# Kernel optimization log

Measured on AMD Instinct MI355X. Metric: run time of the kernel, lower is better.

Reference implementation:

```python
import jax, jax.numpy as jnp
import numpy as np

D_MODEL = 768
N_HEADS = 12
D_FF = 3072
EPS = 1e-5


def _dense_params(key, d_in, d_out):
    kw, kb = jax.random.split(key)
    bound = 1.0 / np.sqrt(d_in)
    W = jax.random.uniform(kw, (d_in, d_out), minval=-bound, maxval=bound, dtype=jnp.float32)
    b = jax.random.uniform(kb, (d_out,), minval=-bound, maxval=bound, dtype=jnp.float32)
    return W, b


def setup_inputs() -> dict:
    key = jax.random.key(0)
    ks = jax.random.split(key, 8)
    x = jax.random.normal(ks[0], (2, 2048, D_MODEL), dtype=jnp.float32)
    wq, bq = _dense_params(ks[1], D_MODEL, D_MODEL)
    wk, bk = _dense_params(ks[2], D_MODEL, D_MODEL)
    wv, bv = _dense_params(ks[3], D_MODEL, D_MODEL)
    wo, bo = _dense_params(ks[4], D_MODEL, D_MODEL)
    w1, b1 = _dense_params(ks[5], D_MODEL, D_FF)
    w2, b2 = _dense_params(ks[6], D_FF, D_MODEL)
    g1 = jnp.ones((D_MODEL,), jnp.float32); be1 = jnp.zeros((D_MODEL,), jnp.float32)
    g2 = jnp.ones((D_MODEL,), jnp.float32); be2 = jnp.zeros((D_MODEL,), jnp.float32)
    return {"x": x, "wq": wq, "bq": bq, "wk": wk, "bk": bk, "wv": wv, "bv": bv,
            "wo": wo, "bo": bo, "w1": w1, "b1": b1, "w2": w2, "b2": b2,
            "g1": g1, "be1": be1, "g2": g2, "be2": be2}


def _layernorm(x, g, b):
    mu = jnp.mean(x, axis=-1, keepdims=True)
    var = jnp.mean(jnp.square(x - mu), axis=-1, keepdims=True)
    return (x - mu) * jax.lax.rsqrt(var + EPS) * g + b


def reference(x, wq, bq, wk, bk, wv, bv, wo, bo, w1, b1, w2, b2, g1, be1, g2, be2):
    B, S, D = x.shape
    H, dk = N_HEADS, D // N_HEADS
    # projections -> [B, H, S, dk]
    def split_heads(t):
        return t.reshape(B, S, H, dk).transpose(0, 2, 1, 3)
    q = split_heads(x @ wq + bq)
    k = split_heads(x @ wk + bk)
    v = split_heads(x @ wv + bv)
    scores = jnp.einsum('bhqd,bhkd->bhqk', q, k) / np.sqrt(dk).astype(np.float32)
    causal = jnp.tril(jnp.ones((S, S), dtype=bool))  # True = keep
    scores = jnp.where(causal, scores, -jnp.inf)
    attn = jax.nn.softmax(scores, axis=-1)
    out = jnp.einsum('bhqk,bhkd->bhqd', attn, v)
    out = out.transpose(0, 2, 1, 3).reshape(B, S, D)
    attn_out = out @ wo + bo
    x = _layernorm(x + attn_out, g1, be1)
    ff = jax.nn.relu(x @ w1 + b1) @ w2 + b2
    x = _layernorm(x + ff, g2, be2)
    return x
```

## Files before the change

### kernel.cpp

```cpp
#include <hip/hip_runtime.h>
#include <stdint.h>

#define S_LEN 2048
#define BATCH 2
#define DM 768
#define NH 12
#define DKH 64
#define DFF 3072
#define MROWS (BATCH * S_LEN)

typedef short bf16x8 __attribute__((ext_vector_type(8)));
typedef float f32x4 __attribute__((ext_vector_type(4)));
typedef float f32x16 __attribute__((ext_vector_type(16)));

__device__ __forceinline__ unsigned short f2b(float f) {
    union { float f; unsigned u; } cv; cv.f = f;
    unsigned u = cv.u;
    unsigned r = (u + 0x7FFFu + ((u >> 16) & 1u)) >> 16;
    return (unsigned short)r;
}

__device__ __forceinline__ void gload16(const void* g, void* l) {
    __builtin_amdgcn_global_load_lds(
        (const __attribute__((address_space(1))) unsigned int*)g,
        (__attribute__((address_space(3))) unsigned int*)l, 16, 0, 0);
}

__device__ __forceinline__ unsigned cvtpk(float lo, float hi) {
    unsigned r;
    asm("v_cvt_pk_bf16_f32 %0, %1, %2" : "=v"(r) : "v"(lo), "v"(hi));
    return r;
}
__device__ __forceinline__ void pswap(unsigned &a, unsigned &b) {
    asm("v_permlane32_swap_b32 %0, %1" : "+v"(a), "+v"(b));
}
__device__ __forceinline__ bf16x8 mkpa(unsigned w0, unsigned w1, unsigned w2, unsigned w3) {
    union { unsigned u[4]; bf16x8 h; } cv;
    cv.u[0] = w0; cv.u[1] = w1; cv.u[2] = w2; cv.u[3] = w3;
    return cv.h;
}

__global__ __launch_bounds__(256) void prep_kernel(
    const float* __restrict__ x,
    const float* __restrict__ wq, const float* __restrict__ wk,
    const float* __restrict__ wv, const float* __restrict__ wo,
    const float* __restrict__ w1, const float* __restrict__ w2,
    unsigned short* __restrict__ x16, unsigned short* __restrict__ wqkv16,
    unsigned short* __restrict__ wo16, unsigned short* __restrict__ w116,
    unsigned short* __restrict__ w216) {
    const int t = threadIdx.x;
    int bid = blockIdx.x;
    if (bid < 3072) {
        const int i = bid * 256 + t;
        float4 v = reinterpret_cast<const float4*>(x)[i];
        ushort4 o;
        o.x = f2b(v.x); o.y = f2b(v.y); o.z = f2b(v.z); o.w = f2b(v.w);
        reinterpret_cast<ushort4*>(x16)[i] = o;
        return;
    }
    bid -= 3072;
    const float* in; unsigned short* out; int R, C, bx, by;
    if (bid < 2304) {
        const int wsel = bid / 576, r = bid % 576;
        in = (wsel == 0) ? wq : (wsel == 1) ? wk : (wsel == 2) ? wv : wo;
        out = (wsel == 3) ? wo16 : wqkv16 + (size_t)wsel * DM * DM;
        R = DM; C = DM; bx = r % 24; by = r / 24;
    } else if (bid < 4608) {
        const int r = bid - 2304;
        in = w1; out = w116; R = DM; C = DFF; bx = r % 96; by = r / 96;
    } else {
        const int r = bid - 4608;
        in = w2; out = w216; R = DFF; C = DM; bx = r % 24; by = r / 24;
    }
    __shared__ float tile[32][33];
    const int c0 = bx * 32, r0 = by * 32;
    const int tx = t & 31, ty = t >> 5;
    #pragma unroll
    for (int i = ty; i < 32; i += 8)
        tile[i][tx] = in[(size_t)(r0 + i) * C + c0 + tx];
    __syncthreads();
    #pragma unroll
    for (int i = ty; i < 32; i += 8)
        out[(size_t)(c0 + i) * R + r0 + tx] = f2b(tile[tx][i]);
}

#define STG192(buf, kt)                                                                  \
    {                                                                                    \
        const char* ga = (const char*)(A + (size_t)bm * lda + koff + ((kt) << 6));       \
        const char* gb = (const char*)(Bt + (size_t)bn * ldb + koff + ((kt) << 6));      \
        char* la = (char*)Sh + (buf) * 57344 + t * 16;                                   \
        char* lb = (char*)Sh + (buf) * 57344 + 32768 + t * 16;                           \
        _Pragma("unroll")                                                                \
        for (int p = 0; p < 4; ++p)                                                      \
            gload16(ga + (size_t)(sr + p * 64) * la2 + scb_sw, la + p * 8192);           \
        _Pragma("unroll")                                                                \
        for (int p = 0; p < 3; ++p)                                                      \
            gload16(gb + (size_t)(sr + p * 64) * lb2 + scb_sw, lb + p * 8192);           \
    }

template <int EPI>
__global__ __launch_bounds__(512, 2) void gemm192(
    const unsigned short* __restrict__ A, int lda,
    const unsigned short* __restrict__ Bt, int ldb,
    const float* __restrict__ bias0, const float* __restrict__ bias1,
    const float* __restrict__ bias2,
    unsigned short* __restrict__ ob0, unsigned short* __restrict__ ob1,
    unsigned short* __restrict__ ob2, float* __restrict__ of,
    int M, int N, int Ksub, float qscale) {
    __shared__ __align__(16) unsigned short Sh[2 * 28672];
    const int t = threadIdx.x;
    const int wave = t >> 6, lane = t & 63;
    const int wr = wave >> 2, wc = wave & 3;
    const int bn = blockIdx.x * 192, bm = blockIdx.y * 256;
    const int koff = (EPI == 2) ? blockIdx.z * Ksub : 0;
    const int lr = lane & 15;
    const int lk8 = (lane >> 4) << 3;
    const int sr = t >> 3;
    const int scb = (t & 7) * 16;
    const int scb_sw = scb ^ ((sr & 7) << 4);
    const int swr = (lr & 7) << 4;
    const size_t la2 = (size_t)lda * 2, lb2 = (size_t)ldb * 2;

    f32x4 acc[8][3];
    #pragma unroll
    for (int i = 0; i < 8; ++i)
        #pragma unroll
        for (int j = 0; j < 3; ++j) { f32x4 z = {0.f, 0.f, 0.f, 0.f}; acc[i][j] = z; }

    const int nkt = Ksub >> 6;
    STG192(0, 0)
    for (int kt = 0; kt < nkt; ++kt) {
        const int cur = kt & 1;
        if (kt + 1 < nkt) {
            STG192(cur ^ 1, kt + 1)
            asm volatile("s_waitcnt vmcnt(7)" ::: "memory");
        } else {
            asm volatile("s_waitcnt vmcnt(0)" ::: "memory");
        }
        __builtin_amdgcn_s_barrier();
        __builtin_amdgcn_sched_barrier(0);
        const char* Ab = (const char*)Sh + cur * 57344;
        const char* Bb = Ab + 32768;
        #pragma unroll
        for (int ks = 0; ks < 64; ks += 32) {
            const int cbsw = ((ks + lk8) * 2) ^ swr;
            bf16x8 af[8], bfv[3];
            #pragma unroll
            for (int i = 0; i < 8; ++i)
                af[i] = *reinterpret_cast<const bf16x8*>(Ab + (wr * 128 + i * 16 + lr) * 128 + cbsw);
            #pragma unroll
            for (int j = 0; j < 3; ++j)
                bfv[j] = *reinterpret_cast<const bf16x8*>(Bb + (wc * 48 + j * 16 + lr) * 128 + cbsw);
            __builtin_amdgcn_s_setprio(1);
            #pragma unroll
            for (int i = 0; i < 8; ++i)
                #pragma unroll
                for (int j = 0; j < 3; ++j)
                    acc[i][j] = __builtin_amdgcn_mfma_f32_16x16x32_bf16(af[i], bfv[j], acc[i][j], 0, 0, 0);
            __builtin_amdgcn_s_setprio(0);
        }
        __builtin_amdgcn_s_barrier();
    }

    const int r0 = (lane >> 4) << 2;
    if (EPI == 0) {
        #pragma unroll
        for (int i = 0; i < 8; ++i) {
            const int row_b = bm + wr * 128 + i * 16 + r0;
            #pragma unroll
            for (int j = 0; j < 3; ++j) {
                const int col = bn + wc * 48 + j * 16 + lr;
                const float bvv = bias0[col];
                #pragma unroll
                for (int r = 0; r < 4; ++r) {
                    float vv = acc[i][j][r] + bvv;
                    vv = vv > 0.f ? vv : 0.f;
                    ob0[(size_t)(row_b + r) * N + col] = f2b(vv);
                }
            }
        }
    } else if (EPI == 1) {
        const int sec = (bn >= 2 * DM) ? 2 : (bn >= DM ? 1 : 0);
        const int nb = bn - sec * DM;
        const float* bias = (sec == 0) ? bias0 : (sec == 1 ? bias1 : bias2);
        #pragma unroll
        for (int i = 0; i < 8; ++i) {
            const int row_b = bm + wr * 128 + i * 16 + r0;
            const int b = row_b >> 11, s = row_b & 2047;
            #pragma unroll
            for (int j = 0; j < 3; ++j) {
                const int c768 = nb + wc * 48 + j * 16 + lr;
                const int h = c768 >> 6, d = c768 & 63;
                const float bvv = bias[c768];
                if (sec == 2) {
                    ushort4 w;
                    w.x = f2b(acc[i][j][0] + bvv);
                    w.y = f2b(acc[i][j][1] + bvv);
                    w.z = f2b(acc[i][j][2] + bvv);
                    w.w = f2b(acc[i][j][3] + bvv);
                    *reinterpret_cast<ushort4*>(
                        ob2 + (((size_t)(b * NH + h) * DKH) + d) * S_LEN + s) = w;
                } else {
                    const float sc = (sec == 0) ? qscale : 1.f;
                    unsigned short* dst = (sec == 0) ? ob0 : ob1;
                    #pragma unroll
                    for (int r = 0; r < 4; ++r)
                        dst[(((size_t)(b * NH + h) * S_LEN) + s + r) * DKH + d] =
                            f2b((acc[i][j][r] + bvv) * sc);
                }
            }
        }
    } else {
        float* op = of + (size_t)blockIdx.z * M * N;
        #pragma unroll
        for (int i = 0; i < 8; ++i) {
            const int row_b = bm + wr * 128 + i * 16 + r0;
            #pragma unroll
            for (int j = 0; j < 3; ++j) {
                const int col = bn + wc * 48 + j * 16 + lr;
                #pragma unroll
                for (int r = 0; r < 4; ++r)
                    op[(size_t)(row_b + r) * N + col] = acc[i][j][r];
            }
        }
    }
}

template <int RELU, int RES, int EF32, int EB16>
__global__ __launch_bounds__(256) void gemm_bt64(
    const unsigned short* __restrict__ A, const unsigned short* __restrict__ Bt,
    const float* __restrict__ bias, const float* __restrict__ res,
    float* __restrict__ outf, unsigned short* __restrict__ outb,
    int M, int N, int K) {
    __shared__ __align__(16) unsigned short As[128 * 64];
    __shared__ __align__(16) unsigned short Bs[64 * 64];
    const int t = threadIdx.x;
    const int wave = t >> 6, lane = t & 63;
    const int bn = blockIdx.x * 64, bm = blockIdx.y * 128;
    const int lr = lane & 15;
    const int lk8 = (lane >> 4) << 3;
    const int srow = t >> 3;
    const int scol = (t & 7) * 16;
    f32x4 acc[2][4];
    #pragma unroll
    for (int i = 0; i < 2; ++i)
        #pragma unroll
        for (int j = 0; j < 4; ++j) { f32x4 z = {0.f, 0.f, 0.f, 0.f}; acc[i][j] = z; }
    const int nkt = K >> 6;
    for (int kt = 0; kt < nkt; ++kt) {
        const char* ga = (const char*)(A + (size_t)bm * K + (kt << 6));
        const char* gb = (const char*)(Bt + (size_t)bn * K + (kt << 6));
        const size_t K2 = (size_t)K * 2;
        #pragma unroll
        for (int p = 0; p < 4; ++p)
            gload16(ga + (size_t)(srow + p * 32) * K2 + scol, (char*)As + p * 4096 + t * 16);
        #pragma unroll
        for (int p = 0; p < 2; ++p)
            gload16(gb + (size_t)(srow + p * 32) * K2 + scol, (char*)Bs + p * 4096 + t * 16);
        __syncthreads();
        #pragma unroll
        for (int ks = 0; ks < 64; ks += 32) {
            bf16x8 af[2], bfv[4];
            #pragma unroll
            for (int i = 0; i < 2; ++i)
                af[i] = *reinterpret_cast<const bf16x8*>(&As[(wave * 32 + i * 16 + lr) * 64 + ks + lk8]);
            #pragma unroll
            for (int j = 0; j < 4; ++j)
                bfv[j] = *reinterpret_cast<const bf16x8*>(&Bs[(j * 16 + lr) * 64 + ks + lk8]);
            #pragma unroll
            for (int i = 0; i < 2; ++i)
                #pragma unroll
                for (int j = 0; j < 4; ++j)
                    acc[i][j] = __builtin_amdgcn_mfma_f32_16x16x32_bf16(af[i], bfv[j], acc[i][j], 0, 0, 0);
        }
        __syncthreads();
    }
    const int r0 = (lane >> 4) << 2;
    #pragma unroll
    for (int i = 0; i < 2; ++i) {
        const int row_b = bm + wave * 32 + i * 16 + r0;
        #pragma unroll
        for (int j = 0; j < 4; ++j) {
            const int col = bn + j * 16 + lr;
            const float bvv = bias[col];
            #pragma unroll
            for (int r = 0; r < 4; ++r) {
                float vv = acc[i][j][r] + bvv;
                if (RES) vv += res[(size_t)(row_b + r) * N + col];
                if (RELU) vv = vv > 0.f ? vv : 0.f;
                if (EF32) outf[(size_t)(row_b + r) * N + col] = vv;
                if (EB16) outb[(size_t)(row_b + r) * N + col] = f2b(vv);
            }
        }
    }
}

#define ALOADK(dst, k0v)                                                     \
    _Pragma("unroll") for (int kh = 0; kh < 2; ++kh)                         \
        _Pragma("unroll") for (int c = 0; c < 4; ++c)                        \
            dst[kh][c] = *reinterpret_cast<const bf16x8*>(                   \
                kb + (size_t)((k0v) + kh * 32 + x) * DKH + c * 16 + k8);
#define ALOADV(dst, k0v)                                                     \
    _Pragma("unroll") for (int dt = 0; dt < 2; ++dt)                         \
        _Pragma("unroll") for (int s = 0; s < 4; ++s)                        \
            dst[dt][s] = *reinterpret_cast<const bf16x8*>(                   \
                vbg + (size_t)(dt * 32 + x) * S_LEN + (k0v) + s * 16 + k8);

__global__ __launch_bounds__(64) void attn_mfma_kernel(
    const unsigned short* __restrict__ q16,
    const unsigned short* __restrict__ k16,
    const unsigned short* __restrict__ vt16,
    unsigned short* __restrict__ ctx16) {
    const int lane = threadIdx.x & 63;
    const int bh = blockIdx.x;
    const int qb = (gridDim.y - 1) - blockIdx.y;
    const int b = bh / NH, h = bh % NH;
    const size_t hbase = (size_t)bh * S_LEN * DKH;
    const int x = lane & 31;
    const int hi = lane >> 5;
    const int k8 = hi << 3;
    const int sW = qb << 5;
    const int qg = sW + x;

    bf16x8 qa[4];
    #pragma unroll
    for (int c = 0; c < 4; ++c)
        qa[c] = *reinterpret_cast<const bf16x8*>(
            q16 + hbase + (size_t)(sW + x) * DKH + c * 16 + k8);

    float mst = -3e38f, lst = 0.f;
    f32x16 acc0, acc1;
    #pragma unroll
    for (int r = 0; r < 16; ++r) { acc0[r] = 0.f; acc1[r] = 0.f; }

    const unsigned short* kb = k16 + hbase;
    const unsigned short* vbg = vt16 + hbase;
    const int nt = (sW >> 6) + 1;

    bf16x8 kac[2][4];
    ALOADK(kac, 0)
    for (int kt = 0; kt < nt; ++kt) {
        const int k0 = kt << 6;
        bf16x8 vac[2][4];
        ALOADV(vac, k0)
        bf16x8 kan[2][4];
        if (kt + 1 < nt) { ALOADK(kan, k0 + 64) }

        f32x16 sc0, sc1;
        #pragma unroll
        for (int r = 0; r < 16; ++r) { sc0[r] = 0.f; sc1[r] = 0.f; }
        __builtin_amdgcn_s_setprio(1);
        #pragma unroll
        for (int c = 0; c < 4; ++c) {
            sc0 = __builtin_amdgcn_mfma_f32_32x32x16_bf16(kac[0][c], qa[c], sc0, 0, 0, 0);
            sc1 = __builtin_amdgcn_mfma_f32_32x32x16_bf16(kac[1][c], qa[c], sc1, 0, 0, 0);
        }
        __builtin_amdgcn_s_setprio(0);

        if (kt == nt - 1) {
            #pragma unroll
            for (int r = 0; r < 16; ++r) {
                const int cr = (r & 3) + (hi << 2) + ((r >> 2) << 3);
                if (k0 + cr > qg) sc0[r] = -3e38f;
                if (k0 + 32 + cr > qg) sc1[r] = -3e38f;
            }
        }

        float tm = fmaxf(sc0[0], sc0[1]);
        #pragma unroll
        for (int r = 2; r < 16; ++r) tm = fmaxf(tm, sc0[r]);
        #pragma unroll
        for (int r = 0; r < 16; ++r) tm = fmaxf(tm, sc1[r]);
        tm = fmaxf(tm, __shfl_xor(tm, 32));

        if (!__all(tm <= mst + 8.f)) {
            const float mn = fmaxf(mst, tm);
            const float corr = exp2f(mst - mn);
            mst = mn;
            lst *= corr;
            float cw[16];
            #pragma unroll
            for (int r = 0; r < 16; ++r)
                cw[r] = __shfl(corr, (r & 3) + (hi << 2) + ((r >> 2) << 3));
            #pragma unroll
            for (int r = 0; r < 16; ++r) { acc0[r] *= cw[r]; acc1[r] *= cw[r]; }
        }

        float ts = 0.f;
        #pragma unroll
        for (int r = 0; r < 16; ++r) {
            sc0[r] = exp2f(sc0[r] - mst); ts += sc0[r];
            sc1[r] = exp2f(sc1[r] - mst); ts += sc1[r];
        }
        ts += __shfl_xor(ts, 32);
        lst += ts;

        unsigned a0 = cvtpk(sc0[0], sc0[1]),   b0 = cvtpk(sc0[4], sc0[5]);   pswap(a0, b0);
        unsigned a1 = cvtpk(sc0[2], sc0[3]),   b1 = cvtpk(sc0[6], sc0[7]);   pswap(a1, b1);
        unsigned a2 = cvtpk(sc0[8], sc0[9]),   b2 = cvtpk(sc0[12], sc0[13]); pswap(a2, b2);
        unsigned a3 = cvtpk(sc0[10], sc0[11]), b3 = cvtpk(sc0[14], sc0[15]); pswap(a3, b3);
        bf16x8 pa00 = mkpa(a0, a1, b0, b1);
        bf16x8 pa01 = mkpa(a2, a3, b2, b3);
        unsigned c0 = cvtpk(sc1[0], sc1[1]),   d0 = cvtpk(sc1[4], sc1[5]);   pswap(c0, d0);
        unsigned c1 = cvtpk(sc1[2], sc1[3]),   d1 = cvtpk(sc1[6], sc1[7]);   pswap(c1, d1);
        unsigned c2 = cvtpk(sc1[8], sc1[9]),   d2 = cvtpk(sc1[12], sc1[13]); pswap(c2, d2);
        unsigned c3 = cvtpk(sc1[10], sc1[11]), d3 = cvtpk(sc1[14], sc1[15]); pswap(c3, d3);
        bf16x8 pa10 = mkpa(c0, c1, d0, d1);
        bf16x8 pa11 = mkpa(c2, c3, d2, d3);

        __builtin_amdgcn_s_setprio(1);
        acc0 = __builtin_amdgcn_mfma_f32_32x32x16_bf16(pa00, vac[0][0], acc0, 0, 0, 0);
        acc1 = __builtin_amdgcn_mfma_f32_32x32x16_bf16(pa00, vac[1][0], acc1, 0, 0, 0);
        acc0 = __builtin_amdgcn_mfma_f32_32x32x16_bf16(pa01, vac[0][1], acc0, 0, 0, 0);
        acc1 = __builtin_amdgcn_mfma_f32_32x32x16_bf16(pa01, vac[1][1], acc1, 0, 0, 0);
        acc0 = __builtin_amdgcn_mfma_f32_32x32x16_bf16(pa10, vac[0][2], acc0, 0, 0, 0);
        acc1 = __builtin_amdgcn_mfma_f32_32x32x16_bf16(pa10, vac[1][2], acc1, 0, 0, 0);
        acc0 = __builtin_amdgcn_mfma_f32_32x32x16_bf16(pa11, vac[0][3], acc0, 0, 0, 0);
        acc1 = __builtin_amdgcn_mfma_f32_32x32x16_bf16(pa11, vac[1][3], acc1, 0, 0, 0);
        __builtin_amdgcn_s_setprio(0);

        if (kt + 1 < nt) {
            #pragma unroll
            for (int kh = 0; kh < 2; ++kh)
                #pragma unroll
                for (int c = 0; c < 4; ++c) kac[kh][c] = kan[kh][c];
        }
    }

    const float li = 1.f / lst;
    float lw[16];
    #pragma unroll
    for (int r = 0; r < 16; ++r)
        lw[r] = __shfl(li, (r & 3) + (hi << 2) + ((r >> 2) << 3));
    #pragma unroll
    for (int r = 0; r < 16; ++r) {
        const int q = sW + (r & 3) + (hi << 2) + ((r >> 2) << 3);
        const size_t rowb = ((size_t)b * S_LEN + q) * DM + h * DKH;
        ctx16[rowb + x] = f2b(acc0[r] * lw[r]);
        ctx16[rowb + 32 + x] = f2b(acc1[r] * lw[r]);
    }
}

template <int EB16>
__global__ __launch_bounds__(256) void layernorm_kernel(
    const float* __restrict__ in, const float* __restrict__ gam, const float* __restrict__ bet,
    float* __restrict__ outf, unsigned short* __restrict__ outb) {
    __shared__ float red[8];
    const int row = blockIdx.x, t = threadIdx.x;
    const int wave = t >> 6, lane = t & 63;
    const float* p = in + (size_t)row * DM;
    const float v0 = p[t], v1 = p[t + 256], v2 = p[t + 512];
    float s = v0 + v1 + v2;
    float sq = v0 * v0 + v1 * v1 + v2 * v2;
    #pragma unroll
    for (int off = 32; off > 0; off >>= 1) { s += __shfl_xor(s, off); sq += __shfl_xor(sq, off); }
    if (lane == 0) { red[wave] = s; red[wave + 4] = sq; }
    __syncthreads();
    s = red[0] + red[1] + red[2] + red[3];
    sq = red[4] + red[5] + red[6] + red[7];
    const float mu = s * (1.f / DM);
    const float var = sq * (1.f / DM) - mu * mu;
    const float rs = rsqrtf(var + 1e-5f);
    #pragma unroll
    for (int i = 0; i < 3; ++i) {
        const int c = t + i * 256;
        const float vv = (i == 0 ? v0 : (i == 1 ? v1 : v2));
        const float y = (vv - mu) * rs * gam[c] + bet[c];
        outf[(size_t)row * DM + c] = y;
        if (EB16) outb[(size_t)row * DM + c] = f2b(y);
    }
}

template <int EB16>
__global__ __launch_bounds__(192) void ln_merge_kernel(
    const float* __restrict__ part, size_t pstride, int ns,
    const float* __restrict__ res, const float* __restrict__ bias,
    const float* __restrict__ gam, const float* __restrict__ bet,
    float* __restrict__ outf, unsigned short* __restrict__ outb) {
    __shared__ float red[8];
    const int row = blockIdx.x, t = threadIdx.x;
    const int wave = t >> 6, lane = t & 63;
    const size_t base = (size_t)row * DM;
    float4 v = reinterpret_cast<const float4*>(res + base)[t];
    const float4 bv = reinterpret_cast<const float4*>(bias)[t];
    v.x += bv.x; v.y += bv.y; v.z += bv.z; v.w += bv.w;
    for (int z = 0; z < ns; ++z) {
        const float4 p = reinterpret_cast<const float4*>(part + (size_t)z * pstride + base)[t];
        v.x += p.x; v.y += p.y; v.z += p.z; v.w += p.w;
    }
    float s = v.x + v.y + v.z + v.w;
    float sq = v.x * v.x + v.y * v.y + v.z * v.z + v.w * v.w;
    #pragma unroll
    for (int off = 32; off > 0; off >>= 1) { s += __shfl_xor(s, off); sq += __shfl_xor(sq, off); }
    if (lane == 0) { red[wave] = s; red[wave + 4] = sq; }
    __syncthreads();
    s = red[0] + red[1] + red[2];
    sq = red[4] + red[5] + red[6];
    const float mu = s * (1.f / DM);
    const float var = sq * (1.f / DM) - mu * mu;
    const float rs = rsqrtf(var + 1e-5f);
    const float4 g = reinterpret_cast<const float4*>(gam)[t];
    const float4 be = reinterpret_cast<const float4*>(bet)[t];
    float4 o;
    o.x = (v.x - mu) * rs * g.x + be.x;
    o.y = (v.y - mu) * rs * g.y + be.y;
    o.z = (v.z - mu) * rs * g.z + be.z;
    o.w = (v.w - mu) * rs * g.w + be.w;
    reinterpret_cast<float4*>(outf + base)[t] = o;
    if (EB16) {
        ushort4 ob;
        ob.x = f2b(o.x); ob.y = f2b(o.y); ob.z = f2b(o.z); ob.w = f2b(o.w);
        reinterpret_cast<ushort4*>(outb + base)[t] = ob;
    }
}

extern "C" void kernel_launch(void* const* d_in, const int* in_sizes, int n_in,
                              void* d_out, int out_size, void* d_ws, size_t ws_size,
                              hipStream_t stream) {
    const float* x   = (const float*)d_in[0];
    const float* wq  = (const float*)d_in[1];
    const float* bq  = (const float*)d_in[2];
    const float* wk  = (const float*)d_in[3];
    const float* bk  = (const float*)d_in[4];
    const float* wv  = (const float*)d_in[5];
    const float* bv  = (const float*)d_in[6];
    const float* wo  = (const float*)d_in[7];
    const float* bo  = (const float*)d_in[8];
    const float* w1  = (const float*)d_in[9];
    const float* b1  = (const float*)d_in[10];
    const float* w2  = (const float*)d_in[11];
    const float* b2  = (const float*)d_in[12];
    const float* g1  = (const float*)d_in[13];
    const float* be1 = (const float*)d_in[14];
    const float* g2  = (const float*)d_in[15];
    const float* be2 = (const float*)d_in[16];

    char* wp = (char*)d_ws;
    auto alloc = [&](size_t bytes) -> void* {
        void* r = (void*)wp;
        wp += (bytes + 255) & ~(size_t)255;
        return r;
    };
    const int M = MROWS;
    unsigned short* wqkv16 = (unsigned short*)alloc((size_t)3 * DM * DM * 2);
    unsigned short* wo16 = (unsigned short*)alloc((size_t)DM * DM * 2);
    unsigned short* w116 = (unsigned short*)alloc((size_t)DM * DFF * 2);
    unsigned short* w216 = (unsigned short*)alloc((size_t)DM * DFF * 2);
    unsigned short* ctx16 = (unsigned short*)alloc((size_t)M * DM * 2);
    float* y1 = (float*)alloc((size_t)M * DM * 4);
    unsigned short* x16  = (unsigned short*)alloc((size_t)M * DM * 2);
    unsigned short* q16  = (unsigned short*)alloc((size_t)M * DM * 2);
    unsigned short* k16  = (unsigned short*)alloc((size_t)M * DM * 2);
    unsigned short* vt16 = (unsigned short*)alloc((size_t)M * DM * 2);
    unsigned short* ff116 = x16;
    unsigned short* x116  = ctx16;

    const size_t per = (size_t)M * DM * 4;
    size_t used = (size_t)(wp - (char*)d_ws);
    int NS = 1;
    if (used + 4 * per + 1024 <= ws_size) NS = 4;
    else if (used + 2 * per + 1024 <= ws_size) NS = 2;
    float* part = (float*)alloc((size_t)NS * per);

    prep_kernel<<<9984, 256, 0, stream>>>(x, wq, wk, wv, wo, w1, w2,
                                          x16, wqkv16, wo16, w116, w216);

    const float QSCALE = 0.125f * 1.44269504088896f;
    gemm192<1><<<dim3(3 * DM / 192, M / 256), 512, 0, stream>>>(
        x16, DM, wqkv16, DM, bq, bk, bv, q16, k16, vt16, nullptr, M, 3 * DM, DM, QSCALE);

    attn_mfma_kernel<<<dim3(BATCH * NH, S_LEN / 32), 64, 0, stream>>>(q16, k16, vt16, ctx16);

    gemm_bt64<0, 1, 1, 0><<<dim3(DM / 64, M / 128), 256, 0, stream>>>(
        ctx16, wo16, bo, x, y1, nullptr, M, DM, DM);
    layernorm_kernel<1><<<M, 256, 0, stream>>>(y1, g1, be1, y1, x116);

    gemm192<0><<<dim3(DFF / 192, M / 256), 512, 0, stream>>>(
        x116, DM, w116, DM, b1, nullptr, nullptr, ff116, nullptr, nullptr, nullptr, M, DFF, DM, 1.f);

    gemm192<2><<<dim3(DM / 192, M / 256, NS), 512, 0, stream>>>(
        ff116, DFF, w216, DFF, nullptr, nullptr, nullptr, nullptr, nullptr, nullptr, part,
        M, DM, DFF / NS, 1.f);
    ln_merge_kernel<0><<<M, 192, 0, stream>>>(part, per / 4, NS, y1, b2, g2, be2,
                                              (float*)d_out, nullptr);
}
```

Measured before the change: 187.6 us.

## Split attention KV range across two blocks and merge partials

```diff
diff --git a/kernel.cpp b/kernel.cpp
--- a/kernel.cpp
+++ b/kernel.cpp
@@ -8,6 +8,7 @@
 #define DKH 64
 #define DFF 3072
 #define MROWS (BATCH * S_LEN)
+#define NBH (BATCH * NH)
 
 typedef short bf16x8 __attribute__((ext_vector_type(8)));
 typedef float f32x4 __attribute__((ext_vector_type(4)));
@@ -310,11 +311,12 @@
     const unsigned short* __restrict__ q16,
     const unsigned short* __restrict__ k16,
     const unsigned short* __restrict__ vt16,
-    unsigned short* __restrict__ ctx16) {
+    float* __restrict__ Op,
+    float* __restrict__ mlp) {
     const int lane = threadIdx.x & 63;
     const int bh = blockIdx.x;
     const int qb = (gridDim.y - 1) - blockIdx.y;
-    const int b = bh / NH, h = bh % NH;
+    const int cz = blockIdx.z;
     const size_t hbase = (size_t)bh * S_LEN * DKH;
     const int x = lane & 31;
     const int hi = lane >> 5;
@@ -336,15 +338,18 @@
     const unsigned short* kb = k16 + hbase;
     const unsigned short* vbg = vt16 + hbase;
     const int nt = (sW >> 6) + 1;
+    const int h1 = (nt + 1) >> 1;
+    const int kt0 = cz ? h1 : 0;
+    const int kt1 = cz ? nt : h1;
 
     bf16x8 kac[2][4];
-    ALOADK(kac, 0)
-    for (int kt = 0; kt < nt; ++kt) {
+    if (kt0 < kt1) { ALOADK(kac, kt0 << 6) }
+    for (int kt = kt0; kt < kt1; ++kt) {
         const int k0 = kt << 6;
         bf16x8 vac[2][4];
         ALOADV(vac, k0)
         bf16x8 kan[2][4];
-        if (kt + 1 < nt) { ALOADK(kan, k0 + 64) }
+        if (kt + 1 < kt1) { ALOADK(kan, (kt + 1) << 6) }
 
         f32x16 sc0, sc1;
         #pragma unroll
@@ -419,7 +424,7 @@
         acc1 = __builtin_amdgcn_mfma_f32_32x32x16_bf16(pa11, vac[1][3], acc1, 0, 0, 0);
         __builtin_amdgcn_s_setprio(0);
 
-        if (kt + 1 < nt) {
+        if (kt + 1 < kt1) {
             #pragma unroll
             for (int kh = 0; kh < 2; ++kh)
                 #pragma unroll
@@ -427,18 +432,40 @@
         }
     }
 
-    const float li = 1.f / lst;
-    float lw[16];
-    #pragma unroll
-    for (int r = 0; r < 16; ++r)
-        lw[r] = __shfl(li, (r & 3) + (hi << 2) + ((r >> 2) << 3));
+    const size_t cb = (size_t)(cz * NBH + bh);
+    float* Oq = Op + (cb * S_LEN + sW) * 64;
     #pragma unroll
     for (int r = 0; r < 16; ++r) {
-        const int q = sW + (r & 3) + (hi << 2) + ((r >> 2) << 3);
-        const size_t rowb = ((size_t)b * S_LEN + q) * DM + h * DKH;
-        ctx16[rowb + x] = f2b(acc0[r] * lw[r]);
-        ctx16[rowb + 32 + x] = f2b(acc1[r] * lw[r]);
-    }
+        const int cr = (r & 3) + (hi << 2) + ((r >> 2) << 3);
+        Oq[(size_t)cr * 64 + x] = acc0[r];
+        Oq[(size_t)cr * 64 + 32 + x] = acc1[r];
+    }
+    if (lane < 32)
+        reinterpret_cast<float2*>(mlp)[cb * S_LEN + sW + lane] = make_float2(mst, lst);
+}
+
+__global__ __launch_bounds__(256) void attn_merge_kernel(
+    const float* __restrict__ Op, const float* __restrict__ mlp,
+    unsigned short* __restrict__ ctx16) {
+    const int t = threadIdx.x;
+    const int r = blockIdx.x * 16 + (t >> 4);
+    const int l16 = t & 15;
+    const int bh = r >> 11, s = r & 2047;
+    const int b = bh / NH, h = bh % NH;
+    const float2 ml0 = reinterpret_cast<const float2*>(mlp)[r];
+    const float2 ml1 = reinterpret_cast<const float2*>(mlp)[NBH * S_LEN + r];
+    const float m = fmaxf(ml0.x, ml1.x);
+    const float a = exp2f(ml0.x - m), bb = exp2f(ml1.x - m);
+    const float li = 1.f / (ml0.y * a + ml1.y * bb);
+    const float4 o0 = reinterpret_cast<const float4*>(Op + (size_t)r * 64)[l16];
+    const float4 o1 = reinterpret_cast<const float4*>(Op + ((size_t)NBH * S_LEN + r) * 64)[l16];
+    ushort4 w;
+    w.x = f2b((o0.x * a + o1.x * bb) * li);
+    w.y = f2b((o0.y * a + o1.y * bb) * li);
+    w.z = f2b((o0.z * a + o1.z * bb) * li);
+    w.w = f2b((o0.w * a + o1.w * bb) * li);
+    *reinterpret_cast<ushort4*>(
+        ctx16 + ((size_t)(b * S_LEN + s)) * DM + h * DKH + l16 * 4) = w;
 }
 
 template <int EB16>
@@ -552,6 +579,7 @@
     unsigned short* q16  = (unsigned short*)alloc((size_t)M * DM * 2);
     unsigned short* k16  = (unsigned short*)alloc((size_t)M * DM * 2);
     unsigned short* vt16 = (unsigned short*)alloc((size_t)M * DM * 2);
+    float* mlbuf = (float*)alloc((size_t)2 * NBH * S_LEN * 2 * 4);
     unsigned short* ff116 = x16;
     unsigned short* x116  = ctx16;
 
@@ -560,7 +588,8 @@
     int NS = 1;
     if (used + 4 * per + 1024 <= ws_size) NS = 4;
     else if (used + 2 * per + 1024 <= ws_size) NS = 2;
-    float* part = (float*)alloc((size_t)NS * per);
+    float* part = (float*)alloc((size_t)(NS < 2 ? 2 : NS) * per);
+    float* Opart = part;
 
     prep_kernel<<<9984, 256, 0, stream>>>(x, wq, wk, wv, wo, w1, w2,
                                           x16, wqkv16, wo16, w116, w216);
@@ -569,7 +598,9 @@
     gemm192<1><<<dim3(3 * DM / 192, M / 256), 512, 0, stream>>>(
         x16, DM, wqkv16, DM, bq, bk, bv, q16, k16, vt16, nullptr, M, 3 * DM, DM, QSCALE);
 
-    attn_mfma_kernel<<<dim3(BATCH * NH, S_LEN / 32), 64, 0, stream>>>(q16, k16, vt16, ctx16);
+    attn_mfma_kernel<<<dim3(NBH, S_LEN / 32, 2), 64, 0, stream>>>(
+        q16, k16, vt16, Opart, mlbuf);
+    attn_merge_kernel<<<NBH * S_LEN / 16, 256, 0, stream>>>(Opart, mlbuf, ctx16);
 
     gemm_bt64<0, 1, 1, 0><<<dim3(DM / 64, M / 128), 256, 0, stream>>>(
         ctx16, wo16, bo, x, y1, nullptr, M, DM, DM);
```

New measurement: 194.1 us. +3.5%, slower.

## Stage attention K/V tiles through double-buffered swizzled LDS via async global-to-LDS loads

Applied to the files above, without the earlier changes.

```diff
diff --git a/kernel.cpp b/kernel.cpp
--- a/kernel.cpp
+++ b/kernel.cpp
@@ -8,6 +8,7 @@
 #define DKH 64
 #define DFF 3072
 #define MROWS (BATCH * S_LEN)
+#define NBH (BATCH * NH)
 
 typedef short bf16x8 __attribute__((ext_vector_type(8)));
 typedef float f32x4 __attribute__((ext_vector_type(4)));
@@ -295,22 +296,26 @@
     }
 }
 
-#define ALOADK(dst, k0v)                                                     \
-    _Pragma("unroll") for (int kh = 0; kh < 2; ++kh)                         \
-        _Pragma("unroll") for (int c = 0; c < 4; ++c)                        \
-            dst[kh][c] = *reinterpret_cast<const bf16x8*>(                   \
-                kb + (size_t)((k0v) + kh * 32 + x) * DKH + c * 16 + k8);
-#define ALOADV(dst, k0v)                                                     \
-    _Pragma("unroll") for (int dt = 0; dt < 2; ++dt)                         \
-        _Pragma("unroll") for (int s = 0; s < 4; ++s)                        \
-            dst[dt][s] = *reinterpret_cast<const bf16x8*>(                   \
-                vbg + (size_t)(dt * 32 + x) * S_LEN + (k0v) + s * 16 + k8);
+#define STAGEKV(buf, kt)                                                              \
+    {                                                                                 \
+        const char* kg = kbyte + (((size_t)(kt)) << 13);                              \
+        const char* vg = vbyte + (((size_t)(kt)) << 7);                               \
+        char* lk = (char*)&KV[buf][0][0] + lane * 16;                                 \
+        char* lv = (char*)&KV[buf][1][0] + lane * 16;                                 \
+        _Pragma("unroll")                                                             \
+        for (int i = 0; i < 8; ++i)                                                   \
+            gload16(kg + (i * 8 + sub) * 128 + ccs, lk + i * 1024);                   \
+        _Pragma("unroll")                                                             \
+        for (int i = 0; i < 8; ++i)                                                   \
+            gload16(vg + (size_t)(i * 8 + sub) * (S_LEN * 2) + ccs, lv + i * 1024);   \
+    }
 
 __global__ __launch_bounds__(64) void attn_mfma_kernel(
     const unsigned short* __restrict__ q16,
     const unsigned short* __restrict__ k16,
     const unsigned short* __restrict__ vt16,
     unsigned short* __restrict__ ctx16) {
+    __shared__ __align__(16) char KV[2][2][8192];
     const int lane = threadIdx.x & 63;
     const int bh = blockIdx.x;
     const int qb = (gridDim.y - 1) - blockIdx.y;
@@ -321,6 +326,9 @@
     const int k8 = hi << 3;
     const int sW = qb << 5;
     const int qg = sW + x;
+    const int sub = lane >> 3;
+    const int ccs = ((lane & 7) * 16) ^ (sub << 4);
+    const int swz = (x & 7) << 4;
 
     bf16x8 qa[4];
     #pragma unroll
@@ -333,18 +341,26 @@
     #pragma unroll
     for (int r = 0; r < 16; ++r) { acc0[r] = 0.f; acc1[r] = 0.f; }
 
-    const unsigned short* kb = k16 + hbase;
-    const unsigned short* vbg = vt16 + hbase;
+    const char* kbyte = (const char*)(k16 + hbase);
+    const char* vbyte = (const char*)(vt16 + hbase);
     const int nt = (sW >> 6) + 1;
 
-    bf16x8 kac[2][4];
-    ALOADK(kac, 0)
+    STAGEKV(0, 0)
     for (int kt = 0; kt < nt; ++kt) {
+        const int cur = kt & 1;
+        asm volatile("s_waitcnt vmcnt(0)" ::: "memory");
+        if (kt + 1 < nt) STAGEKV(cur ^ 1, kt + 1)
+        const char* Kb = (const char*)&KV[cur][0][0];
+        const char* Vb = (const char*)&KV[cur][1][0];
         const int k0 = kt << 6;
-        bf16x8 vac[2][4];
-        ALOADV(vac, k0)
-        bf16x8 kan[2][4];
-        if (kt + 1 < nt) { ALOADK(kan, k0 + 64) }
+
+        bf16x8 kaf[2][4];
+        #pragma unroll
+        for (int kh = 0; kh < 2; ++kh)
+            #pragma unroll
+            for (int c = 0; c < 4; ++c)
+                kaf[kh][c] = *reinterpret_cast<const bf16x8*>(
+                    Kb + (kh * 32 + x) * 128 + ((c * 32 + hi * 16) ^ swz));
 
         f32x16 sc0, sc1;
         #pragma unroll
@@ -352,8 +368,8 @@
         __builtin_amdgcn_s_setprio(1);
         #pragma unroll
         for (int c = 0; c < 4; ++c) {
-            sc0 = __builtin_amdgcn_mfma_f32_32x32x16_bf16(kac[0][c], qa[c], sc0, 0, 0, 0);
-            sc1 = __builtin_amdgcn_mfma_f32_32x32x16_bf16(kac[1][c], qa[c], sc1, 0, 0, 0);
+            sc0 = __builtin_amdgcn_mfma_f32_32x32x16_bf16(kaf[0][c], qa[c], sc0, 0, 0, 0);
+            sc1 = __builtin_amdgcn_mfma_f32_32x32x16_bf16(kaf[1][c], qa[c], sc1, 0, 0, 0);
         }
         __builtin_amdgcn_s_setprio(0);
 
@@ -408,23 +424,24 @@
         bf16x8 pa10 = mkpa(c0, c1, d0, d1);
         bf16x8 pa11 = mkpa(c2, c3, d2, d3);
 
+        bf16x8 vaf[2][4];
+        #pragma unroll
+        for (int dt = 0; dt < 2; ++dt)
+            #pragma unroll
+            for (int s = 0; s < 4; ++s)
+                vaf[dt][s] = *reinterpret_cast<const bf16x8*>(
+                    Vb + (dt * 32 + x) * 128 + ((s * 32 + hi * 16) ^ swz));
+
         __builtin_amdgcn_s_setprio(1);
-        acc0 = __builtin_amdgcn_mfma_f32_32x32x16_bf16(pa00, vac[0][0], acc0, 0, 0, 0);
-        acc1 = __builtin_amdgcn_mfma_f32_32x32x16_bf16(pa00, vac[1][0], acc1, 0, 0, 0);
-        acc0 = __builtin_amdgcn_mfma_f32_32x32x16_bf16(pa01, vac[0][1], acc0, 0, 0, 0);
-        acc1 = __builtin_amdgcn_mfma_f32_32x32x16_bf16(pa01, vac[1][1], acc1, 0, 0, 0);
-        acc0 = __builtin_amdgcn_mfma_f32_32x32x16_bf16(pa10, vac[0][2], acc0, 0, 0, 0);
-        acc1 = __builtin_amdgcn_mfma_f32_32x32x16_bf16(pa10, vac[1][2], acc1, 0, 0, 0);
-        acc0 = __builtin_amdgcn_mfma_f32_32x32x16_bf16(pa11, vac[0][3], acc0, 0, 0, 0);
-        acc1 = __builtin_amdgcn_mfma_f32_32x32x16_bf16(pa11, vac[1][3], acc1, 0, 0, 0);
+        acc0 = __builtin_amdgcn_mfma_f32_32x32x16_bf16(pa00, vaf[0][0], acc0, 0, 0, 0);
+        acc1 = __builtin_amdgcn_mfma_f32_32x32x16_bf16(pa00, vaf[1][0], acc1, 0, 0, 0);
+        acc0 = __builtin_amdgcn_mfma_f32_32x32x16_bf16(pa01, vaf[0][1], acc0, 0, 0, 0);
+        acc1 = __builtin_amdgcn_mfma_f32_32x32x16_bf16(pa01, vaf[1][1], acc1, 0, 0, 0);
+        acc0 = __builtin_amdgcn_mfma_f32_32x32x16_bf16(pa10, vaf[0][2], acc0, 0, 0, 0);
+        acc1 = __builtin_amdgcn_mfma_f32_32x32x16_bf16(pa10, vaf[1][2], acc1, 0, 0, 0);
+        acc0 = __builtin_amdgcn_mfma_f32_32x32x16_bf16(pa11, vaf[0][3], acc0, 0, 0, 0);
+        acc1 = __builtin_amdgcn_mfma_f32_32x32x16_bf16(pa11, vaf[1][3], acc1, 0, 0, 0);
         __builtin_amdgcn_s_setprio(0);
-
-        if (kt + 1 < nt) {
-            #pragma unroll
-            for (int kh = 0; kh < 2; ++kh)
-                #pragma unroll
-                for (int c = 0; c < 4; ++c) kac[kh][c] = kan[kh][c];
-        }
     }
 
     const float li = 1.f / lst;
@@ -569,7 +586,7 @@
     gemm192<1><<<dim3(3 * DM / 192, M / 256), 512, 0, stream>>>(
         x16, DM, wqkv16, DM, bq, bk, bv, q16, k16, vt16, nullptr, M, 3 * DM, DM, QSCALE);
 
-    attn_mfma_kernel<<<dim3(BATCH * NH, S_LEN / 32), 64, 0, stream>>>(q16, k16, vt16, ctx16);
+    attn_mfma_kernel<<<dim3(NBH, S_LEN / 32), 64, 0, stream>>>(q16, k16, vt16, ctx16);
 
     gemm_bt64<0, 1, 1, 0><<<dim3(DM / 64, M / 128), 256, 0, stream>>>(
         ctx16, wo16, bo, x, y1, nullptr, M, DM, DM);
```

New measurement: 184.2 us. Within noise of the previous version (-1.8%).
